# Optimization experiments

Hardware: AMD Instinct MI355X
Metric: run time of the kernel (lower is better)

Reference implementation:

```python
import jax, jax.numpy as jnp
import numpy as np

DIM = 192
HRES, WRES = 64, 64
NUM_HEADS = 6
WS = 8  # window_size
MLP_HIDDEN = int(DIM * 4.0)
EPS = 1e-5


def layer_norm(x, gamma, beta):
    mu = jnp.mean(x, axis=-1, keepdims=True)
    var = jnp.var(x, axis=-1, keepdims=True)
    return (x - mu) * jax.lax.rsqrt(var + EPS) * gamma + beta


def window_partition(x, ws):
    B, H, W, C = x.shape
    x = x.reshape(B, H // ws, ws, W // ws, ws, C)
    x = jnp.transpose(x, (0, 1, 3, 2, 4, 5))
    return x.reshape(-1, ws * ws, C)


def window_reverse(windows, ws, H, W, C):
    B = windows.shape[0] // ((H // ws) * (W // ws))
    x = windows.reshape(B, H // ws, W // ws, ws, ws, C)
    x = jnp.transpose(x, (0, 1, 3, 2, 4, 5))
    return x.reshape(B, H, W, C)


def setup_inputs() -> dict:
    key = jax.random.key(0)
    ks = jax.random.split(key, 12)
    s = 0.02
    return {
        "x": jax.random.normal(ks[0], (32, HRES * WRES, DIM), dtype=jnp.float32),
        "norm1_g": jnp.ones((DIM,), jnp.float32),
        "norm1_b": jnp.zeros((DIM,), jnp.float32),
        "qkv_w": jax.random.normal(ks[1], (DIM, 3 * DIM), jnp.float32) * s,
        "qkv_b": jnp.zeros((3 * DIM,), jnp.float32),
        "proj_w": jax.random.normal(ks[2], (DIM, DIM), jnp.float32) * s,
        "proj_b": jnp.zeros((DIM,), jnp.float32),
        "norm2_g": jnp.ones((DIM,), jnp.float32),
        "norm2_b": jnp.zeros((DIM,), jnp.float32),
        "fc1_w": jax.random.normal(ks[3], (DIM, MLP_HIDDEN), jnp.float32) * s,
        "fc1_b": jnp.zeros((MLP_HIDDEN,), jnp.float32),
        "fc2_w": jax.random.normal(ks[4], (MLP_HIDDEN, DIM), jnp.float32) * s,
        "fc2_b": jnp.zeros((DIM,), jnp.float32),
    }


def reference(x, norm1_g, norm1_b, qkv_w, qkv_b, proj_w, proj_b,
              norm2_g, norm2_b, fc1_w, fc1_b, fc2_w, fc2_b):
    B, L, C = x.shape
    H, W = HRES, WRES
    hd = C // NUM_HEADS
    scale = hd ** -0.5

    shortcut = x
    h = layer_norm(x, norm1_g, norm1_b).reshape(B, H, W, C)
    win = window_partition(h, WS)  # [nW*B, WS*WS, C]
    Bw, N, _ = win.shape

    qkv = (win @ qkv_w + qkv_b).reshape(Bw, N, 3, NUM_HEADS, hd)
    q, k, v = jnp.transpose(qkv, (2, 0, 3, 1, 4))  # each [Bw, H, N, hd]
    attn = jnp.einsum('bhnd,bhmd->bhnm', q, k) * scale
    attn = jax.nn.softmax(attn, axis=-1)
    out = jnp.einsum('bhnm,bhmd->bhnd', attn, v)
    out = jnp.transpose(out, (0, 2, 1, 3)).reshape(Bw, N, C)
    out = out @ proj_w + proj_b

    h = window_reverse(out, WS, H, W, C).reshape(B, L, C)
    x = shortcut + h

    m = layer_norm(x, norm2_g, norm2_b)
    m = jax.nn.gelu(m @ fc1_w + fc1_b, approximate=False)
    m = m @ fc2_w + fc2_b
    return x + m
```

## Files before the change

### kernel.cpp

```cpp
#include <hip/hip_runtime.h>
#include <hip/hip_bf16.h>
#include <math.h>

#define DIM   192
#define NH    6
#define HD    32
#define WSZ   8
#define HRES_ 64
#define WRES_ 64
#define BATCH 32
#define LTOK  (HRES_*WRES_)
#define MTOK  (BATCH*LTOK)
#define QKVN  (3*DIM)
#define MLPH  (4*DIM)

using bf16 = __hip_bfloat16;
using bf16x8 = __attribute__((ext_vector_type(8))) short;
using f32x4  = __attribute__((ext_vector_type(4))) float;

__device__ __forceinline__ float bf2f(bf16 h) { return __bfloat162float(h); }
__device__ __forceinline__ float us2f(unsigned short u) {
    union { unsigned u32; float f; } c; c.u32 = ((unsigned)u) << 16; return c.f;
}

__global__ void detect_kernel(const unsigned short* __restrict__ g, int* __restrict__ flag)
{
    *flag = (g[0] == 0x3F80) ? 0 : 1;
}

__global__ __launch_bounds__(256) void cvt_kernel(
    const void* __restrict__ src, bf16* __restrict__ dst,
    long n, long elem_off, const int* __restrict__ flag)
{
    long i = ((long)blockIdx.x * 256 + threadIdx.x) * 8;
    if (i >= n) return;
    if (i + 8 <= n) {
        if (*flag) {
            const float* s = (const float*)src + elem_off + i;
            float4 a = *reinterpret_cast<const float4*>(s);
            float4 b = *reinterpret_cast<const float4*>(s + 4);
            bf16 o[8];
            o[0]=__float2bfloat16(a.x); o[1]=__float2bfloat16(a.y);
            o[2]=__float2bfloat16(a.z); o[3]=__float2bfloat16(a.w);
            o[4]=__float2bfloat16(b.x); o[5]=__float2bfloat16(b.y);
            o[6]=__float2bfloat16(b.z); o[7]=__float2bfloat16(b.w);
            *reinterpret_cast<bf16x8*>(dst + i) = *reinterpret_cast<const bf16x8*>(o);
        } else {
            *reinterpret_cast<bf16x8*>(dst + i) =
                *reinterpret_cast<const bf16x8*>((const bf16*)src + elem_off + i);
        }
    } else {
        for (long k2 = i; k2 < n; ++k2) {
            if (*flag) dst[k2] = __float2bfloat16(((const float*)src)[elem_off + k2]);
            else       dst[k2] = ((const bf16*)src)[elem_off + k2];
        }
    }
}

__global__ __launch_bounds__(256) void store_kernel(
    const bf16* __restrict__ src, void* __restrict__ dst,
    long n, long elem_off, const int* __restrict__ flag)
{
    long i = ((long)blockIdx.x * 256 + threadIdx.x) * 8;
    if (i >= n) return;
    if (i + 8 <= n) {
        bf16x8 v = *reinterpret_cast<const bf16x8*>(src + i);
        if (*flag) {
            float* d = (float*)dst + elem_off + i;
            float4 a, b;
            a.x = us2f((unsigned short)v[0]); a.y = us2f((unsigned short)v[1]);
            a.z = us2f((unsigned short)v[2]); a.w = us2f((unsigned short)v[3]);
            b.x = us2f((unsigned short)v[4]); b.y = us2f((unsigned short)v[5]);
            b.z = us2f((unsigned short)v[6]); b.w = us2f((unsigned short)v[7]);
            *reinterpret_cast<float4*>(d)     = a;
            *reinterpret_cast<float4*>(d + 4) = b;
        } else {
            *reinterpret_cast<bf16x8*>((bf16*)dst + elem_off + i) = v;
        }
    } else {
        for (long k2 = i; k2 < n; ++k2) {
            if (*flag) ((float*)dst)[elem_off + k2] = bf2f(src[k2]);
            else       ((bf16*)dst)[elem_off + k2] = src[k2];
        }
    }
}

__global__ __launch_bounds__(256) void ln_kernel(
    const bf16* __restrict__ x, const bf16* __restrict__ g,
    const bf16* __restrict__ b, bf16* __restrict__ y)
{
    int wave = threadIdx.x >> 6;
    int lane = threadIdx.x & 63;
    long token = (long)blockIdx.x * 4 + wave;
    const bf16* xp = x + token * DIM;
    float f0 = bf2f(xp[lane]);
    float f1 = bf2f(xp[lane + 64]);
    float f2 = bf2f(xp[lane + 128]);
    float s  = f0 + f1 + f2;
    float ss = f0*f0 + f1*f1 + f2*f2;
    #pragma unroll
    for (int m = 1; m < 64; m <<= 1) { s += __shfl_xor(s, m); ss += __shfl_xor(ss, m); }
    float mean = s * (1.0f/192.0f);
    float var  = ss * (1.0f/192.0f) - mean*mean;
    float rstd = rsqrtf(var + 1e-5f);
    bf16* yp = y + token * DIM;
    yp[lane]       = __float2bfloat16((f0-mean)*rstd*bf2f(g[lane])       + bf2f(b[lane]));
    yp[lane + 64]  = __float2bfloat16((f1-mean)*rstd*bf2f(g[lane + 64])  + bf2f(b[lane + 64]));
    yp[lane + 128] = __float2bfloat16((f2-mean)*rstd*bf2f(g[lane + 128]) + bf2f(b[lane + 128]));
}

__global__ void transpose_kernel(const bf16* __restrict__ in, bf16* __restrict__ out,
                                 int K, int N)
{
    int idx = blockIdx.x * 256 + threadIdx.x;
    if (idx < K * N) {
        int n = idx % N, k = idx / N;
        out[n * K + k] = in[idx];
    }
}

template<int EPI>
__global__ __launch_bounds__(256) void gemm_bt(
    const bf16* __restrict__ A, const bf16* __restrict__ Bt,
    const bf16* __restrict__ bias, const bf16* __restrict__ res,
    bf16* __restrict__ C, int M, int N, int K)
{
    constexpr int KC = 192;
    __shared__ __align__(16) bf16 bsh[(KC/32) * 4 * 64 * 8];
    int tid  = threadIdx.x;
    int wave = tid >> 6, lane = tid & 63;
    int t = lane & 15, q = lane >> 4;
    int  n0 = blockIdx.x * 64;
    long m0 = (long)blockIdx.y * 128;

    f32x4 acc[2][4] = {};

    for (int kc = 0; kc < K; kc += KC) {
        __syncthreads();
        for (int s = tid; s < (KC/32) * 256; s += 256) {
            int ks  = s >> 8;
            int rem = s & 255;
            int j   = rem >> 6;
            int ln  = rem & 63;
            int tt = ln & 15, qq = ln >> 4;
            int n = j * 16 + tt;
            int k = ks * 32 + qq * 8;
            const float4* src = reinterpret_cast<const float4*>(
                Bt + (long)(n0 + n) * K + kc + k);
            reinterpret_cast<float4*>(bsh)[s] = *src;
        }
        __syncthreads();

        const bf16* arow = A + (m0 + wave * 32 + t) * (long)K + kc + q * 8;
        #pragma unroll
        for (int ks = 0; ks < KC/32; ++ks) {
            bf16x8 a0 = *reinterpret_cast<const bf16x8*>(arow + ks * 32);
            bf16x8 a1 = *reinterpret_cast<const bf16x8*>(arow + 16 * (long)K + ks * 32);
            #pragma unroll
            for (int j = 0; j < 4; ++j) {
                bf16x8 b = reinterpret_cast<const bf16x8*>(bsh)[ks * 256 + j * 64 + lane];
                acc[0][j] = __builtin_amdgcn_mfma_f32_16x16x32_bf16(a0, b, acc[0][j], 0, 0, 0);
                acc[1][j] = __builtin_amdgcn_mfma_f32_16x16x32_bf16(a1, b, acc[1][j], 0, 0, 0);
            }
        }
    }

    #pragma unroll
    for (int j = 0; j < 4; ++j) {
        int col = n0 + j * 16 + t;
        float bv = bf2f(bias[col]);
        #pragma unroll
        for (int i = 0; i < 2; ++i) {
            #pragma unroll
            for (int r = 0; r < 4; ++r) {
                long row = m0 + wave * 32 + i * 16 + q * 4 + r;
                float v = acc[i][j][r] + bv;
                if (EPI == 1) v = v * 0.5f * (1.0f + erff(v * 0.70710678118f));
                if (EPI == 2) v += bf2f(res[row * N + col]);
                C[row * N + col] = __float2bfloat16(v);
            }
        }
    }
}

__global__ __launch_bounds__(256) void attn_kernel(
    const bf16* __restrict__ qkv, bf16* __restrict__ out)
{
    int win  = blockIdx.x;
    int head = blockIdx.y;
    __shared__ __align__(16) bf16 qs[64 * 32];
    __shared__ __align__(16) bf16 ksm[64 * 32];
    __shared__ __align__(16) bf16 vt[32 * 64];
    __shared__ __align__(16) bf16 ps[64 * 64];
    __shared__ int nat[64];

    int tid  = threadIdx.x;
    int wave = tid >> 6, lane = tid & 63;
    int t = lane & 15, q = lane >> 4;

    if (tid < 64) {
        int b = win >> 6;
        int widx = win & 63;
        int wh = widx >> 3, ww = widx & 7;
        int r = wh * 8 + (tid >> 3);
        int c = ww * 8 + (tid & 7);
        nat[tid] = b * LTOK + r * WRES_ + c;
    }
    __syncthreads();

    {
        int token = tid >> 2, ch = tid & 3;
        long base = (long)nat[token] * QKVN + head * HD + ch * 8;
        float4 qv = *reinterpret_cast<const float4*>(qkv + base);
        float4 kv = *reinterpret_cast<const float4*>(qkv + base + DIM);
        float4 vv = *reinterpret_cast<const float4*>(qkv + base + 2 * DIM);
        *reinterpret_cast<float4*>(qs  + token * 32 + ch * 8) = qv;
        *reinterpret_cast<float4*>(ksm + token * 32 + ch * 8) = kv;
        const bf16* vp = reinterpret_cast<const bf16*>(&vv);
        #pragma unroll
        for (int e = 0; e < 8; ++e) vt[(ch * 8 + e) * 64 + token] = vp[e];
    }
    __syncthreads();

    f32x4 sacc[4] = {};
    {
        bf16x8 aq = *reinterpret_cast<const bf16x8*>(qs + (wave * 16 + t) * 32 + q * 8);
        #pragma unroll
        for (int j = 0; j < 4; ++j) {
            bf16x8 bk = *reinterpret_cast<const bf16x8*>(ksm + (j * 16 + t) * 32 + q * 8);
            sacc[j] = __builtin_amdgcn_mfma_f32_16x16x32_bf16(aq, bk, sacc[j], 0, 0, 0);
        }
    }

    const float scale = 0.17677669529663689f;
    #pragma unroll
    for (int r = 0; r < 4; ++r) {
        float m_ = fmaxf(fmaxf(sacc[0][r], sacc[1][r]), fmaxf(sacc[2][r], sacc[3][r]));
        #pragma unroll
        for (int msk = 1; msk < 16; msk <<= 1) m_ = fmaxf(m_, __shfl_xor(m_, msk));
        float p[4], sum = 0.f;
        #pragma unroll
        for (int j = 0; j < 4; ++j) { p[j] = expf((sacc[j][r] - m_) * scale); sum += p[j]; }
        #pragma unroll
        for (int msk = 1; msk < 16; msk <<= 1) sum += __shfl_xor(sum, msk);
        float inv = 1.0f / sum;
        int row = wave * 16 + q * 4 + r;
        #pragma unroll
        for (int j = 0; j < 4; ++j)
            ps[row * 64 + j * 16 + t] = __float2bfloat16(p[j] * inv);
    }
    __syncthreads();

    f32x4 oacc[2] = {};
    #pragma unroll
    for (int kk = 0; kk < 2; ++kk) {
        bf16x8 ap = *reinterpret_cast<const bf16x8*>(ps + (wave * 16 + t) * 64 + kk * 32 + q * 8);
        #pragma unroll
        for (int j = 0; j < 2; ++j) {
            bf16x8 bv = *reinterpret_cast<const bf16x8*>(vt + (j * 16 + t) * 64 + kk * 32 + q * 8);
            oacc[j] = __builtin_amdgcn_mfma_f32_16x16x32_bf16(ap, bv, oacc[j], 0, 0, 0);
        }
    }
    #pragma unroll
    for (int j = 0; j < 2; ++j) {
        #pragma unroll
        for (int r = 0; r < 4; ++r) {
            int row = wave * 16 + q * 4 + r;
            out[(long)nat[row] * DIM + head * HD + j * 16 + t] = __float2bfloat16(oacc[j][r]);
        }
    }
}

extern "C" void kernel_launch(void* const* d_in, const int* in_sizes, int n_in,
                              void* d_out, int out_size, void* d_ws, size_t ws_size,
                              hipStream_t stream)
{
    char* ws = (char*)d_ws;
    size_t off = 0;
    auto alloc = [&](size_t bytes) {
        char* p = ws + off;
        off += (bytes + 255) & ~(size_t)255;
        return p;
    };

    int* flag = (int*)alloc(sizeof(int));

    static const int psz[12] = { DIM, DIM, DIM*QKVN, QKVN, DIM*DIM, DIM,
                                 DIM, DIM, DIM*MLPH, MLPH, MLPH*DIM, DIM };
    bf16* par[12];
    for (int i = 0; i < 12; ++i) par[i] = (bf16*)alloc((size_t)psz[i] * 2);
    bf16 *n1g = par[0], *n1b = par[1], *qkvw = par[2], *qkvb = par[3],
         *projw = par[4], *projb = par[5], *n2g = par[6], *n2b = par[7],
         *fc1w = par[8], *fc1b = par[9], *fc2w = par[10], *fc2b = par[11];

    bf16* wqkv_t  = (bf16*)alloc((size_t)QKVN * DIM * 2);
    bf16* wproj_t = (bf16*)alloc((size_t)DIM * DIM * 2);
    bf16* wfc1_t  = (bf16*)alloc((size_t)MLPH * DIM * 2);
    bf16* wfc2_t  = (bf16*)alloc((size_t)DIM * MLPH * 2);
    size_t fixed_off = off;

    int C = 32;
    while (C > 1) {
        size_t Mc = (size_t)C * LTOK;
        if (fixed_off + Mc * 2688 + 4096 <= ws_size) break;
        C >>= 1;
    }
    size_t Mc = (size_t)C * LTOK;
    bf16* xb = (bf16*)alloc(Mc * 384);
    bf16* R  = (bf16*)alloc(Mc * 384);
    bf16* Y  = (bf16*)alloc(Mc * 384);
    bf16* S  = (bf16*)alloc(Mc * 1536);
    int nchunks = BATCH / C;

    detect_kernel<<<1, 1, 0, stream>>>((const unsigned short*)d_in[1], flag);

    for (int i = 0; i < 12; ++i) {
        unsigned blocks = (unsigned)(((long)psz[i] + 8*256 - 1) / (8*256));
        cvt_kernel<<<blocks, 256, 0, stream>>>(d_in[i + 1], par[i], psz[i], 0, flag);
    }

    transpose_kernel<<<(DIM*QKVN + 255)/256, 256, 0, stream>>>(qkvw, wqkv_t, DIM, QKVN);
    transpose_kernel<<<(DIM*DIM  + 255)/256, 256, 0, stream>>>(projw, wproj_t, DIM, DIM);
    transpose_kernel<<<(DIM*MLPH + 255)/256, 256, 0, stream>>>(fc1w, wfc1_t, DIM, MLPH);
    transpose_kernel<<<(MLPH*DIM + 255)/256, 256, 0, stream>>>(fc2w, wfc2_t, MLPH, DIM);

    for (int ci = 0; ci < nchunks; ++ci) {
        long eoff = (long)ci * Mc * DIM;
        long nelem = (long)Mc * DIM;
        unsigned vblocks = (unsigned)((nelem + 8*256 - 1) / (8*256));

        cvt_kernel<<<vblocks, 256, 0, stream>>>(d_in[0], xb, nelem, eoff, flag);
        ln_kernel<<<(unsigned)(Mc/4), 256, 0, stream>>>(xb, n1g, n1b, R);
        gemm_bt<0><<<dim3(QKVN/64, Mc/128), 256, 0, stream>>>(R, wqkv_t, qkvb, nullptr, S, (int)Mc, QKVN, DIM);
        attn_kernel<<<dim3(C*64, NH), 256, 0, stream>>>(S, R);
        gemm_bt<2><<<dim3(DIM/64, Mc/128), 256, 0, stream>>>(R, wproj_t, projb, xb, Y, (int)Mc, DIM, DIM);
        ln_kernel<<<(unsigned)(Mc/4), 256, 0, stream>>>(Y, n2g, n2b, R);
        gemm_bt<1><<<dim3(MLPH/64, Mc/128), 256, 0, stream>>>(R, wfc1_t, fc1b, nullptr, S, (int)Mc, MLPH, DIM);
        gemm_bt<2><<<dim3(DIM/64, Mc/128), 256, 0, stream>>>(S, wfc2_t, fc2b, Y, Y, (int)Mc, DIM, MLPH);
        store_kernel<<<vblocks, 256, 0, stream>>>(Y, d_out, nelem, eoff, flag);
    }
}
```

Measured before the change: 776.5 us.

## Fuse fc1+GELU+fc2 into one MLP kernel keeping hidden activations in LDS

Replaces the two separate MLP GEMM launches with a single kernel. Each 128-row block computes fc1 plus GELU in 192-column chunks into shared memory and immediately accumulates the fc2 contribution in registers. This removes the write and re-read of the 768-wide hidden activation to global memory and shrinks the workspace, which can allow larger batch chunks. In exchange each block holds 24 accumulator tiles in registers and synchronises frequently, which may reduce occupancy and has no overlap between weight loads and MFMA work.

```diff
diff --git a/kernel.cpp b/kernel.cpp
--- a/kernel.cpp
+++ b/kernel.cpp
@@ -183,6 +183,120 @@
     }
 }
 
+__global__ __launch_bounds__(256) void mlp_kernel(
+    const bf16* __restrict__ A,   const bf16* __restrict__ W1t,
+    const bf16* __restrict__ b1,  const bf16* __restrict__ W2t,
+    const bf16* __restrict__ b2,  const bf16* __restrict__ res,
+    bf16* __restrict__ out, int M)
+{
+    __shared__ __align__(16) bf16 bsh[6 * 4 * 64 * 8];
+    __shared__ __align__(16) bf16 hsh[128 * 200];
+    int tid  = threadIdx.x;
+    int wave = tid >> 6, lane = tid & 63;
+    int t = lane & 15, q = lane >> 4;
+    long m0 = (long)blockIdx.x * 128;
+
+    bf16x8 a_reg[2][6];
+    #pragma unroll
+    for (int i = 0; i < 2; ++i) {
+        const bf16* ap = A + (m0 + wave * 32 + i * 16 + t) * (long)DIM + q * 8;
+        #pragma unroll
+        for (int ks = 0; ks < 6; ++ks)
+            a_reg[i][ks] = *reinterpret_cast<const bf16x8*>(ap + ks * 32);
+    }
+
+    f32x4 oacc[2][12] = {};
+
+    for (int nc = 0; nc < 4; ++nc) {
+        for (int j64 = 0; j64 < 3; ++j64) {
+            __syncthreads();
+            #pragma unroll
+            for (int it = 0; it < 6; ++it) {
+                int s   = it * 256 + tid;
+                int ks  = s >> 8;
+                int rem = s & 255;
+                int j   = rem >> 6;
+                int ln  = rem & 63;
+                int n   = nc * 192 + j64 * 64 + j * 16 + (ln & 15);
+                int k   = ks * 32 + (ln >> 4) * 8;
+                reinterpret_cast<float4*>(bsh)[s] =
+                    *reinterpret_cast<const float4*>(W1t + (long)n * DIM + k);
+            }
+            __syncthreads();
+
+            f32x4 hacc[2][4] = {};
+            #pragma unroll
+            for (int ks = 0; ks < 6; ++ks) {
+                #pragma unroll
+                for (int j = 0; j < 4; ++j) {
+                    bf16x8 b = reinterpret_cast<const bf16x8*>(bsh)[ks * 256 + j * 64 + lane];
+                    hacc[0][j] = __builtin_amdgcn_mfma_f32_16x16x32_bf16(a_reg[0][ks], b, hacc[0][j], 0, 0, 0);
+                    hacc[1][j] = __builtin_amdgcn_mfma_f32_16x16x32_bf16(a_reg[1][ks], b, hacc[1][j], 0, 0, 0);
+                }
+            }
+            #pragma unroll
+            for (int j = 0; j < 4; ++j) {
+                int cl = j64 * 64 + j * 16 + t;
+                float bv = bf2f(b1[nc * 192 + cl]);
+                #pragma unroll
+                for (int i = 0; i < 2; ++i) {
+                    #pragma unroll
+                    for (int r = 0; r < 4; ++r) {
+                        int row = wave * 32 + i * 16 + q * 4 + r;
+                        float v = hacc[i][j][r] + bv;
+                        v = v * 0.5f * (1.0f + erff(v * 0.70710678118f));
+                        hsh[row * 200 + cl] = __float2bfloat16(v);
+                    }
+                }
+            }
+        }
+
+        for (int j64 = 0; j64 < 3; ++j64) {
+            __syncthreads();
+            #pragma unroll
+            for (int it = 0; it < 6; ++it) {
+                int s   = it * 256 + tid;
+                int ks  = s >> 8;
+                int rem = s & 255;
+                int j   = rem >> 6;
+                int ln  = rem & 63;
+                int n   = j64 * 64 + j * 16 + (ln & 15);
+                int k   = nc * 192 + ks * 32 + (ln >> 4) * 8;
+                reinterpret_cast<float4*>(bsh)[s] =
+                    *reinterpret_cast<const float4*>(W2t + (long)n * MLPH + k);
+            }
+            __syncthreads();
+
+            #pragma unroll
+            for (int ks = 0; ks < 6; ++ks) {
+                bf16x8 h0 = *reinterpret_cast<const bf16x8*>(hsh + (wave * 32 + t) * 200 + ks * 32 + q * 8);
+                bf16x8 h1 = *reinterpret_cast<const bf16x8*>(hsh + (wave * 32 + 16 + t) * 200 + ks * 32 + q * 8);
+                #pragma unroll
+                for (int j = 0; j < 4; ++j) {
+                    bf16x8 b = reinterpret_cast<const bf16x8*>(bsh)[ks * 256 + j * 64 + lane];
+                    oacc[0][j64 * 4 + j] = __builtin_amdgcn_mfma_f32_16x16x32_bf16(h0, b, oacc[0][j64 * 4 + j], 0, 0, 0);
+                    oacc[1][j64 * 4 + j] = __builtin_amdgcn_mfma_f32_16x16x32_bf16(h1, b, oacc[1][j64 * 4 + j], 0, 0, 0);
+                }
+            }
+        }
+    }
+
+    #pragma unroll
+    for (int jj = 0; jj < 12; ++jj) {
+        int col = (jj >> 2) * 64 + (jj & 3) * 16 + t;
+        float bv = bf2f(b2[col]);
+        #pragma unroll
+        for (int i = 0; i < 2; ++i) {
+            #pragma unroll
+            for (int r = 0; r < 4; ++r) {
+                long row = m0 + wave * 32 + i * 16 + q * 4 + r;
+                float v = oacc[i][jj][r] + bv + bf2f(res[row * DIM + col]);
+                out[row * DIM + col] = __float2bfloat16(v);
+            }
+        }
+    }
+}
+
 __global__ __launch_bounds__(256) void attn_kernel(
     const bf16* __restrict__ qkv, bf16* __restrict__ out)
 {
@@ -302,14 +416,14 @@
     int C = 32;
     while (C > 1) {
         size_t Mc = (size_t)C * LTOK;
-        if (fixed_off + Mc * 2688 + 4096 <= ws_size) break;
+        if (fixed_off + Mc * 2304 + 4096 <= ws_size) break;
         C >>= 1;
     }
     size_t Mc = (size_t)C * LTOK;
     bf16* xb = (bf16*)alloc(Mc * 384);
     bf16* R  = (bf16*)alloc(Mc * 384);
     bf16* Y  = (bf16*)alloc(Mc * 384);
-    bf16* S  = (bf16*)alloc(Mc * 1536);
+    bf16* S  = (bf16*)alloc(Mc * 1152);
     int nchunks = BATCH / C;
 
     detect_kernel<<<1, 1, 0, stream>>>((const unsigned short*)d_in[1], flag);
@@ -335,8 +449,7 @@
         attn_kernel<<<dim3(C*64, NH), 256, 0, stream>>>(S, R);
         gemm_bt<2><<<dim3(DIM/64, Mc/128), 256, 0, stream>>>(R, wproj_t, projb, xb, Y, (int)Mc, DIM, DIM);
         ln_kernel<<<(unsigned)(Mc/4), 256, 0, stream>>>(Y, n2g, n2b, R);
-        gemm_bt<1><<<dim3(MLPH/64, Mc/128), 256, 0, stream>>>(R, wfc1_t, fc1b, nullptr, S, (int)Mc, MLPH, DIM);
-        gemm_bt<2><<<dim3(DIM/64, Mc/128), 256, 0, stream>>>(S, wfc2_t, fc2b, Y, Y, (int)Mc, DIM, MLPH);
+        mlp_kernel<<<(unsigned)(Mc/128), 256, 0, stream>>>(R, wfc1_t, fc1b, wfc2_t, fc2b, Y, Y, (int)Mc);
         store_kernel<<<vblocks, 256, 0, stream>>>(Y, d_out, nelem, eoff, flag);
     }
 }
```

Result: slower. 810.1 us (+4.3%).
